# Performance work log

Measured on AMD Instinct MI355X. Metric: run time of the kernel, lower is better.

## Reference

```python
import jax, jax.numpy as jnp
import numpy as np

D = 20       # bond_dim (= virtual_dim = per-module output_dim)
BATCH = 128
BN_EPS = 1e-5


def _unfold(t, h, w, n):
    # torch x.unfold(2,h,h).unfold(3,w,w).reshape(b, C, -1, n)
    B, C, H, W = t.shape
    t = t.reshape(B, C, H // h, h, W // w, w).transpose(0, 1, 2, 4, 3, 5)
    return t.reshape(B, C, -1, n)


def _mps(x, cores, label):
    # x: [b, C, P, n] site values; cores: [P, n, D, F, D] with F = 2*C; label: [P, D, O, D]
    feat = jnp.concatenate([x, 1.0 - x], axis=1)              # [b, F, P, n]  ([x, 1-x] feature map)
    M = jnp.einsum('bfpn,pnufv->npbuv', feat, cores)           # [n, P, b, D, D] site matrices
    v = jnp.full((cores.shape[2],), cores.shape[2] ** -0.5, dtype=x.dtype)  # boundary vector
    left = jnp.einsum('u,pbuv->pbv', v, M[0])
    for i in range(1, M.shape[0]):                             # n is small & static (4 or 16)
        left = jnp.einsum('pbu,pbuv->pbv', left, M[i])
    return jnp.einsum('pbu,puov,v->bpo', left, label, v)       # [b, P, O]


def _bn(y, gamma, beta):
    # training-mode BatchNorm1d over channel axis 1 of [b, C, L]
    mean = y.mean(axis=(0, 2), keepdims=True)
    var = y.var(axis=(0, 2), keepdims=True)
    return (y - mean) * jax.lax.rsqrt(var + BN_EPS) * gamma[None, :, None] + beta[None, :, None]


def setup_inputs() -> dict:
    key = jax.random.key(0)
    ks = jax.random.split(key, 9)
    f32 = jnp.float32
    def core(k, shape):
        F = shape[-2]
        return (jax.random.normal(k, shape, f32) * np.float32(np.sqrt(3.0 / (D * F))))
    def lab(k, shape):
        return jax.random.normal(k, shape, f32) * np.float32(D ** -0.5)
    x = jax.random.uniform(ks[0], (BATCH, 48, 32, 32), f32)
    return {
        'x': x,
        'cores1': core(ks[1], (256, 4, D, 96, D)), 'label1': lab(ks[2], (256, D, D, D)),
        'g1': jnp.ones(256, f32), 'b1': jnp.zeros(256, f32),
        'cores2': core(ks[3], (64, 4, D, 2 * D, D)), 'label2': lab(ks[4], (64, D, D, D)),
        'g2': jnp.ones(64, f32), 'b2': jnp.zeros(64, f32),
        'cores3': core(ks[5], (16, 4, D, 2 * D, D)), 'label3': lab(ks[6], (16, D, D, D)),
        'g3': jnp.ones(16, f32), 'b3': jnp.zeros(16, f32),
        'coresF': core(ks[7], (16, D, 2 * D, D)), 'labelF': lab(ks[8], (D, 10, D)),
    }


def reference(x, cores1, label1, g1, b1, cores2, label2, g2, b2,
              cores3, label3, g3, b3, coresF, labelF):
    b = x.shape[0]
    # stage 1: 256 patch-experts over 4 sites each
    x1 = _unfold(x, 16, 16, 4)                  # [b, 48, 256, 4]
    y = _mps(x1, cores1, label1)                # [b, 256, D]
    y = _bn(y, g1, b1).reshape(b, D, 16, 16)    # faithful patch<->bond mixing view
    # stage 2: 64 experts
    y2 = _unfold(y, 8, 8, 4)                    # [b, D, 64, 4]
    y = _mps(y2, cores2, label2)                # [b, 64, D]
    y = _bn(y, g2, b2).reshape(b, D, 8, 8)
    # stage 3: 16 experts
    y3 = _unfold(y, 4, 4, 4)                    # [b, D, 16, 4]
    y = _mps(y3, cores3, label3)                # [b, 16, D]
    y = _bn(y, g3, b3)
    # final MPS over the 16 expert outputs (channels = D)
    y = y.transpose(0, 2, 1)[:, :, None, :]     # [b, D, 1, 16]
    out = _mps(y, coresF[None], labelF[None])   # [b, 1, 10]
    return out[:, 0, :]                         # squeeze -> [b, 10]
```

## Files before the change

### kernel.cpp

```cpp
#include <hip/hip_runtime.h>

#define VB 0.22360679774997896f

typedef __attribute__((ext_vector_type(8))) _Float16 half8;
typedef __attribute__((ext_vector_type(4))) float f32x4;

#define Z1_OFF   0
#define Z2_OFF   655360
#define Z3_OFF   819200
#define GS1_OFF  860160
#define GQ1_OFF  860416
#define GS2_OFF  860672
#define GQ2_OFF  860736
#define GS3_OFF  860800
#define GQ3_OFF  860816
#define LV1_OFF  860832
#define LV2_OFF  963232
#define LV3_OFF  988832
#define WH2_OFF  995232
#define WH3_OFF  4272032

#define WAVEBAR() __builtin_amdgcn_wave_barrier()

__global__ __launch_bounds__(256, 8)
void prep_kernel(const float* __restrict__ c2, const float* __restrict__ c3,
                 const float* __restrict__ l1, const float* __restrict__ l2,
                 const float* __restrict__ l3,
                 _Float16* __restrict__ Wh2, _Float16* __restrict__ Wh3,
                 float* __restrict__ v1, float* __restrict__ v2,
                 float* __restrict__ v3,
                 float* __restrict__ gzero)
{
    const int tid = threadIdx.x;
    const int b   = blockIdx.x;

    if (b < 4000) {
        int gidx = b * 256 + tid;
        int bb = gidx / 640;
        int o  = gidx - bb * 640;
        const float* src;
        _Float16* dst;
        if (bb < 1280) { src = c2 + (size_t)bb * 3200;          dst = Wh2 + (size_t)bb * 5120; }
        else           { src = c3 + (size_t)(bb - 1280) * 3200; dst = Wh3 + (size_t)(bb - 1280) * 5120; }
        int q  = o >> 6, l = o & 63;
        int ks = q / 5, nt = q - ks * 5;
        int c  = nt * 16 + (l & 15);
        int ul = c / 20;
        int v  = c - ul * 20;
        int f0 = ks * 32 + ((l >> 4) << 3);
        half8 hv;
        if (f0 < 40) {
            const float* sp = src + ul * 800 + f0 * 20 + v;
            #pragma unroll
            for (int j = 0; j < 8; ++j) hv[j] = (_Float16)sp[j * 20];
        } else {
            #pragma unroll
            for (int j = 0; j < 8; ++j) hv[j] = (_Float16)0.f;
        }
        *(half8*)(dst + (size_t)o * 8) = hv;
    } else if (b < 4336) {
        const int bb = b - 4000;
        const float* lb;
        float* ov;
        if (bb < 256)      { lb = l1 + (size_t)bb * 8000;         ov = v1 + bb * 400; }
        else if (bb < 320) { lb = l2 + (size_t)(bb - 256) * 8000; ov = v2 + (bb - 256) * 400; }
        else               { lb = l3 + (size_t)(bb - 320) * 8000; ov = v3 + (bb - 320) * 400; }
        for (int i = tid; i < 400; i += 256) {
            const float4* s = (const float4*)(lb + i * 20);
            float acc = 0.f;
            #pragma unroll
            for (int t = 0; t < 5; ++t) {
                float4 w = s[t];
                acc += w.x + w.y + w.z + w.w;
            }
            ov[i] = acc * VB;
        }
    } else {
        for (int i = tid; i < 672; i += 256) gzero[i] = 0.f;
    }
}

#define CHUNKX(ucv, LAST)                                                     \
    {                                                                         \
        if (!(LAST)) {                                                        \
            _Pragma("unroll")                                                 \
            for (int k = 0; k < 4; ++k) {                                     \
                int i4 = tid + k * 512;                                       \
                if (i4 < 1920) wr[k] = *(const float4*)(wnext + i4 * 4);      \
            }                                                                 \
            wnext += 7680;                                                    \
        }                                                                     \
        f32x4 acc[5];                                                         \
        _Pragma("unroll")                                                     \
        for (int nt = 0; nt < 5; ++nt) acc[nt] = (f32x4){0.f, 0.f, 0.f, 0.f};\
        _Pragma("unroll")                                                     \
        for (int ks = 0; ks < 3; ++ks) {                                      \
            _Pragma("unroll")                                                 \
            for (int nt = 0; nt < 5; ++nt) {                                  \
                half8 bf = *(const half8*)&Fcur[((ks * 5 + nt) * 64 + l) * 8];\
                acc[nt] = __builtin_amdgcn_mfma_f32_16x16x32_f16(             \
                    af[ks], bf, acc[nt], 0, 0, 0);                            \
            }                                                                 \
        }                                                                     \
        _Pragma("unroll")                                                     \
        for (int nt = 0; nt < 5; ++nt) {                                      \
            _Pragma("unroll")                                                 \
            for (int r = 0; r < 4; ++r)                                       \
                Mw[(hi * 4 + r) * 84 + nt * 16 + row16] = acc[nt][r];         \
        }                                                                     \
        WAVEBAR();                                                            \
        _Pragma("unroll")                                                     \
        for (int ul = 0; ul < 4; ++ul) {                                      \
            float lvx = lw[bQ * 20 + (ucv) * 4 + ul];                         \
            _Pragma("unroll")                                                 \
            for (int j = 0; j < 5; ++j)                                       \
                lacc[j] += lvx * Mw[bQ * 84 + ul * 20 + mh * 5 + j];          \
        }                                                                     \
        WAVEBAR();                                                            \
        __syncthreads();                                                      \
        if (!(LAST)) {                                                        \
            _Pragma("unroll")                                                 \
            for (int k = 0; k < 4; ++k) {                                     \
                int i4 = tid + k * 512;                                       \
                if (i4 < 1920) {                                              \
                    float vals[4] = {wr[k].x, wr[k].y, wr[k].z, wr[k].w};     \
                    _Pragma("unroll")                                         \
                    for (int t = 0; t < 4; ++t)                               \
                        Fnxt[sAddr[k][t]] = (_Float16)vals[t];                \
                }                                                             \
            }                                                                 \
        }                                                                     \
        __syncthreads();                                                      \
        { _Float16* t_ = Fcur; Fcur = Fnxt; Fnxt = t_; }                      \
    }

__global__ __launch_bounds__(512, 2)
void fused1_kernel(const float* __restrict__ x, const float* __restrict__ cores1,
                   const float* __restrict__ labv,
                   float* __restrict__ z1, float* __restrict__ gs, float* __restrict__ gq)
{
    __shared__ __align__(16) float xS[8 * 768];
    __shared__ __align__(16) _Float16 Fbuf[2][7680];
    __shared__ __align__(16) float MchunkS[8 * 16 * 84];
    __shared__ __align__(16) float leftS[8 * 320];
    __shared__ float redS[16];

    const int tid = threadIdx.x;
    const int bid = blockIdx.x;
    const int p   = (bid & 7) * 32 + (bid >> 3);
    const int wv  = tid >> 6, l = tid & 63;
    float* xSw = xS + wv * 768;
    float* Mw  = MchunkS + wv * 1344;
    float* lw  = leftS + wv * 320;
    const int row16 = l & 15, hi = l >> 4;
    const int bQ = l >> 2,   mh = l & 3;
    const int hh  = (p >> 7) * 16 + ((p >> 2) & 15);
    const int ww0 = ((p >> 6) & 1) * 16 + (p & 3) * 4;

    float4 xr[12];
    #pragma unroll
    for (int k = 0; k < 12; ++k) {
        int idx = l + k * 64;
        int br = idx / 48, c = idx - br * 48;
        xr[k] = *(const float4*)(x + (((size_t)((wv * 16 + br) * 48 + c)) << 10)
                                   + hh * 32 + ww0);
    }

    int sAddr[4][4];
    #pragma unroll
    for (int k = 0; k < 4; ++k) {
        int i4 = tid + k * 512;
        if (i4 < 1920) {
            #pragma unroll
            for (int t = 0; t < 4; ++t) {
                int e = i4 * 4 + t;
                int v = e % 20;
                int r = e / 20;
                int f = r % 96;
                int ul = r / 96;
                int c = ul * 20 + v;
                sAddr[k][t] = (((f >> 5) * 5 + (c >> 4)) * 64 +
                               ((f >> 3) & 3) * 16 + (c & 15)) * 8 + (f & 7);
            }
        }
    }

    #pragma unroll
    for (int j = 0; j < 5; ++j) lw[bQ * 20 + mh * 5 + j] = VB;
    WAVEBAR();

    float lacc[5] = {0.f, 0.f, 0.f, 0.f, 0.f};
    float4 wr[4];
    const float* wnext = cores1 + (size_t)p * 153600;

    #pragma unroll
    for (int k = 0; k < 4; ++k) {
        int i4 = tid + k * 512;
        if (i4 < 1920) wr[k] = *(const float4*)(wnext + i4 * 4);
    }
    wnext += 7680;
    _Float16* Fcur = &Fbuf[0][0];
    _Float16* Fnxt = &Fbuf[1][0];
    #pragma unroll
    for (int k = 0; k < 4; ++k) {
        int i4 = tid + k * 512;
        if (i4 < 1920) {
            float vals[4] = {wr[k].x, wr[k].y, wr[k].z, wr[k].w};
            #pragma unroll
            for (int t = 0; t < 4; ++t)
                Fcur[sAddr[k][t]] = (_Float16)vals[t];
        }
    }
    __syncthreads();

    #pragma unroll 1
    for (int n = 0; n < 4; ++n) {
        #pragma unroll
        for (int k = 0; k < 12; ++k) {
            int idx = l + k * 64;
            float v = (n == 0) ? xr[k].x : (n == 1) ? xr[k].y
                    : (n == 2) ? xr[k].z : xr[k].w;
            xSw[idx] = v;
        }
        WAVEBAR();
        half8 af[3];
        #pragma unroll
        for (int ks = 0; ks < 3; ++ks) {
            int f0 = ks * 32 + hi * 8;
            int cc = (f0 < 48) ? f0 : f0 - 48;
            float4 a  = *(const float4*)&xSw[row16 * 48 + cc];
            float4 b2 = *(const float4*)&xSw[row16 * 48 + cc + 4];
            float vv[8] = {a.x, a.y, a.z, a.w, b2.x, b2.y, b2.z, b2.w};
            bool inv = (f0 >= 48);
            half8 hv;
            #pragma unroll
            for (int j = 0; j < 8; ++j) hv[j] = (_Float16)(inv ? (1.f - vv[j]) : vv[j]);
            af[ks] = hv;
        }
        WAVEBAR();

        const bool last = (n == 3);
        CHUNKX(0, 0)
        CHUNKX(1, 0)
        CHUNKX(2, 0)
        CHUNKX(3, 0)
        CHUNKX(4, last)

        #pragma unroll
        for (int j = 0; j < 5; ++j) { lw[bQ * 20 + mh * 5 + j] = lacc[j]; lacc[j] = 0.f; }
        WAVEBAR();
    }

    const float* lvp = labv + p * 400;
    #pragma unroll
    for (int k = 0; k < 7; ++k) { int i = l + k * 64; if (i < 400) Mw[i] = lvp[i]; }
    WAVEBAR();
    float yv[5] = {0.f, 0.f, 0.f, 0.f, 0.f};
    #pragma unroll
    for (int u = 0; u < 20; ++u) {
        float lu = lw[bQ * 20 + u];
        #pragma unroll
        for (int j = 0; j < 5; ++j) yv[j] += lu * Mw[u * 20 + mh * 5 + j];
    }
    float s = 0.f, s2 = 0.f;
    #pragma unroll
    for (int j = 0; j < 5; ++j) {
        z1[(size_t)(wv * 16 + bQ) * 5120 + p * 20 + mh * 5 + j] = yv[j];
        s += yv[j]; s2 += yv[j] * yv[j];
    }
    #pragma unroll
    for (int off = 32; off > 0; off >>= 1) {
        s  += __shfl_down(s, off);
        s2 += __shfl_down(s2, off);
    }
    if (l == 0) { redS[wv] = s; redS[8 + wv] = s2; }
    __syncthreads();
    if (tid == 0) {
        float S = 0.f, Q = 0.f;
        #pragma unroll
        for (int w2 = 0; w2 < 8; ++w2) { S += redS[w2]; Q += redS[8 + w2]; }
        gs[p] = S; gq[p] = Q;
    }
}

#define UCBODYN(ucv, CUR, NXT)                                                   \
    {                                                                            \
        if ((ucv) < 4) {                                                         \
            const _Float16* bptr = whp + (size_t)((ucv) + 1) * 5120;             \
            _Pragma("unroll")                                                    \
            for (int q = 0; q < 10; ++q)                                         \
                NXT[q] = *(const half8*)(bptr + (q * 64 + l) * 8);               \
        }                                                                        \
        f32x4 acc[5];                                                            \
        _Pragma("unroll")                                                        \
        for (int nt = 0; nt < 5; ++nt) acc[nt] = (f32x4){0.f, 0.f, 0.f, 0.f};    \
        _Pragma("unroll")                                                        \
        for (int ks = 0; ks < 2; ++ks) {                                         \
            _Pragma("unroll")                                                    \
            for (int nt = 0; nt < 5; ++nt)                                       \
                acc[nt] = __builtin_amdgcn_mfma_f32_16x16x32_f16(                \
                    af[ks], CUR[ks * 5 + nt], acc[nt], 0, 0, 0);                 \
        }                                                                        \
        _Pragma("unroll")                                                        \
        for (int nt = 0; nt < 5; ++nt) {                                         \
            _Pragma("unroll")                                                    \
            for (int r = 0; r < 4; ++r)                                          \
                Mw[(hi * 4 + r) * 84 + nt * 16 + row16] = acc[nt][r];            \
        }                                                                        \
        WAVEBAR();                                                               \
        _Pragma("unroll")                                                        \
        for (int ul = 0; ul < 4; ++ul) {                                         \
            float lvx = lw[bQ * 20 + (ucv) * 4 + ul];                            \
            _Pragma("unroll")                                                    \
            for (int j = 0; j < 5; ++j)                                          \
                lacc[j] += lvx * Mw[bQ * 84 + ul * 20 + mh * 5 + j];             \
        }                                                                        \
        WAVEBAR();                                                               \
    }

template <int STAGE>
__global__ __launch_bounds__(256, 2)
void fusedN_kernel(const float* __restrict__ zin, const _Float16* __restrict__ Wh,
                   const float* __restrict__ labv,
                   const float* __restrict__ gsin, const float* __restrict__ gqin,
                   const float* __restrict__ gam,  const float* __restrict__ bet,
                   float* __restrict__ zout,
                   float* __restrict__ gsout, float* __restrict__ gqout)
{
    constexpr int ZIN  = (STAGE == 2) ? 5120 : 1280;
    constexpr int ZOUT = (STAGE == 2) ? 1280 : 320;
    constexpr int JUMP = (STAGE == 2) ? 256 : 64;

    __shared__ __align__(16) float zS[4 * 320];
    __shared__ float scS[4 * 20], shS[4 * 20];
    __shared__ __align__(16) float MchunkS[4 * 16 * 84];
    __shared__ __align__(16) float leftS[4 * 320];

    const int tid = threadIdx.x;
    const int p   = blockIdx.x;
    const int bh  = blockIdx.y;
    const int wv  = tid >> 6, l = tid & 63;
    float* zSw = zS + wv * 320;
    float* scw = scS + wv * 20;
    float* shw = shS + wv * 20;
    float* Mw  = MchunkS + wv * 1344;
    float* lw  = leftS + wv * 320;
    const int row16 = l & 15, hi = l >> 4;
    const int bQ = l >> 2,   mh = l & 3;
    const int bg = bh * 64;

    #pragma unroll
    for (int j = 0; j < 5; ++j) lw[bQ * 20 + mh * 5 + j] = VB;
    WAVEBAR();

    float lacc[5] = {0.f, 0.f, 0.f, 0.f, 0.f};

    #pragma unroll 1
    for (int n = 0; n < 4; ++n) {
        int hh, ww;
        if (STAGE == 2) { hh = (p >> 5) * 8 + ((p >> 1) & 7); ww = ((p >> 4) & 1) * 8 + (p & 1) * 4 + n; }
        else            { hh = (p >> 3) * 4 + (p & 3);        ww = ((p >> 2) & 1) * 4 + n; }
        const int oo = (STAGE == 2) ? (hh * 16 + ww) : (hh * 8 + ww);

        if (l < 20) {
            int ch = (l * JUMP + oo) / 20;
            float mean = gsin[ch] * (1.f / 2560.f);
            float var  = gqin[ch] * (1.f / 2560.f) - mean * mean;
            float rstd = rsqrtf(var + 1e-5f);
            float sc = gam[ch] * rstd;
            scw[l] = sc;
            shw[l] = bet[ch] - mean * sc;
        }
        WAVEBAR();
        #pragma unroll
        for (int q = 0; q < 5; ++q) {
            int d = hi * 5 + q;
            float zraw = zin[(size_t)(bg + wv * 16 + row16) * ZIN + d * JUMP + oo];
            zSw[row16 * 20 + d] = zraw * scw[d] + shw[d];
        }
        WAVEBAR();
        half8 af[2];
        #pragma unroll
        for (int ks = 0; ks < 2; ++ks) {
            int f0 = ks * 32 + hi * 8;
            half8 hv;
            #pragma unroll
            for (int j = 0; j < 8; ++j) {
                int f = f0 + j;
                float val;
                if (f < 20)      val = zSw[row16 * 20 + f];
                else if (f < 40) val = 1.f - zSw[row16 * 20 + f - 20];
                else             val = 0.f;
                hv[j] = (_Float16)val;
            }
            af[ks] = hv;
        }
        WAVEBAR();

        const _Float16* whp = Wh + (size_t)((p * 4 + n) * 5) * 5120;
        half8 bA[10], bB[10];
        {
            #pragma unroll
            for (int q = 0; q < 10; ++q) bA[q] = *(const half8*)(whp + (q * 64 + l) * 8);
        }
        UCBODYN(0, bA, bB)
        UCBODYN(1, bB, bA)
        UCBODYN(2, bA, bB)
        UCBODYN(3, bB, bA)
        UCBODYN(4, bA, bB)

        #pragma unroll
        for (int j = 0; j < 5; ++j) { lw[bQ * 20 + mh * 5 + j] = lacc[j]; lacc[j] = 0.f; }
        WAVEBAR();
    }

    const float* lvp = labv + p * 400;
    #pragma unroll
    for (int k = 0; k < 7; ++k) { int i = l + k * 64; if (i < 400) Mw[i] = lvp[i]; }
    WAVEBAR();
    float yv[5] = {0.f, 0.f, 0.f, 0.f, 0.f};
    #pragma unroll
    for (int u = 0; u < 20; ++u) {
        float lu = lw[bQ * 20 + u];
        #pragma unroll
        for (int j = 0; j < 5; ++j) yv[j] += lu * Mw[u * 20 + mh * 5 + j];
    }
    float s = 0.f, s2 = 0.f;
    #pragma unroll
    for (int j = 0; j < 5; ++j) {
        zout[(size_t)(bg + wv * 16 + bQ) * ZOUT + p * 20 + mh * 5 + j] = yv[j];
        s += yv[j]; s2 += yv[j] * yv[j];
    }
    #pragma unroll
    for (int off = 32; off > 0; off >>= 1) {
        s  += __shfl_down(s, off);
        s2 += __shfl_down(s2, off);
    }
    if (l == 0) { atomicAdd(&gsout[p], s); atomicAdd(&gqout[p], s2); }
}

__global__ __launch_bounds__(256, 4)
void final_kernel(const float* __restrict__ z3,
                  const float* __restrict__ coresF,
                  const float* __restrict__ labelF,
                  const float* __restrict__ g3,
                  const float* __restrict__ b3,
                  const float* __restrict__ gsum3,
                  const float* __restrict__ gsq3,
                  float* __restrict__ out)
{
    __shared__ __align__(16) float fS[16 * 40];
    __shared__ __align__(16) float MS[16 * 400];
    __shared__ float lvS[200];
    __shared__ float scS[16], shS[16];
    __shared__ float leftS[20];

    const int b   = blockIdx.x;
    const int tid = threadIdx.x;

    if (tid < 16) {
        float mean = gsum3[tid] * (1.f / 2560.f);
        float var  = gsq3[tid] * (1.f / 2560.f) - mean * mean;
        float rstd = rsqrtf(var + 1e-5f);
        float sc   = g3[tid] * rstd;
        scS[tid] = sc;
        shS[tid] = b3[tid] - mean * sc;
    }
    __syncthreads();

    for (int i = tid; i < 640; i += 256) {
        int n = i / 40, f = i - n * 40;
        float raw = z3[(size_t)b * 320 + n * 20 + (f % 20)];
        float val = raw * scS[n] + shS[n];
        fS[i] = (f < 20) ? val : (1.f - val);
    }
    for (int i = tid; i < 200; i += 256) {
        int u = i / 10, o = i - u * 10;
        const float* lb = labelF + (size_t)(u * 10 + o) * 20;
        float s = 0.f;
        #pragma unroll
        for (int vv = 0; vv < 20; ++vv) s += lb[vv];
        lvS[i] = s * VB;
    }
    __syncthreads();

    for (int i = tid; i < 6400; i += 256) {
        int n = i / 400, uv = i - n * 400;
        int u = uv / 20, v = uv - u * 20;
        const float* wb = coresF + ((size_t)(n * 20 + u) * 40) * 20 + v;
        const float* fb = fS + n * 40;
        float acc = 0.f;
        #pragma unroll
        for (int f = 0; f < 40; ++f) acc += fb[f] * wb[f * 20];
        MS[i] = acc;
    }
    __syncthreads();

    if (tid < 64) {
        if (tid < 20) leftS[tid] = VB;
        WAVEBAR();
        #pragma unroll 1
        for (int n = 0; n < 16; ++n) {
            float tmp = 0.f;
            if (tid < 20) {
                #pragma unroll
                for (int u = 0; u < 20; ++u) tmp += leftS[u] * MS[n * 400 + u * 20 + tid];
            }
            WAVEBAR();
            if (tid < 20) leftS[tid] = tmp;
            WAVEBAR();
        }
        if (tid < 10) {
            float s = 0.f;
            #pragma unroll
            for (int u = 0; u < 20; ++u) s += leftS[u] * lvS[u * 10 + tid];
            out[b * 10 + tid] = s;
        }
    }
}

extern "C" void kernel_launch(void* const* d_in, const int* in_sizes, int n_in,
                              void* d_out, int out_size, void* d_ws, size_t ws_size,
                              hipStream_t stream)
{
    const float* x      = (const float*)d_in[0];
    const float* cores1 = (const float*)d_in[1];
    const float* label1 = (const float*)d_in[2];
    const float* g1     = (const float*)d_in[3];
    const float* b1     = (const float*)d_in[4];
    const float* cores2 = (const float*)d_in[5];
    const float* label2 = (const float*)d_in[6];
    const float* g2     = (const float*)d_in[7];
    const float* b2     = (const float*)d_in[8];
    const float* cores3 = (const float*)d_in[9];
    const float* label3 = (const float*)d_in[10];
    const float* g3     = (const float*)d_in[11];
    const float* b3     = (const float*)d_in[12];
    const float* coresF = (const float*)d_in[13];
    const float* labelF = (const float*)d_in[14];

    float* ws  = (float*)d_ws;
    float* z1  = ws + Z1_OFF;
    float* z2  = ws + Z2_OFF;
    float* z3  = ws + Z3_OFF;
    float* gs1 = ws + GS1_OFF; float* gq1 = ws + GQ1_OFF;
    float* gs2 = ws + GS2_OFF; float* gq2 = ws + GQ2_OFF;
    float* gs3 = ws + GS3_OFF; float* gq3 = ws + GQ3_OFF;
    float* lv1 = ws + LV1_OFF;
    float* lv2 = ws + LV2_OFF;
    float* lv3 = ws + LV3_OFF;
    _Float16* Wh2 = (_Float16*)(ws + WH2_OFF);
    _Float16* Wh3 = (_Float16*)(ws + WH3_OFF);

    prep_kernel<<<4337, 256, 0, stream>>>(cores2, cores3,
                                          label1, label2, label3,
                                          Wh2, Wh3,
                                          lv1, lv2, lv3, gs1);

    fused1_kernel<<<256, 512, 0, stream>>>(x, cores1, lv1, z1, gs1, gq1);
    fusedN_kernel<2><<<dim3(64, 2), 256, 0, stream>>>(z1, Wh2, lv2, gs1, gq1, g1, b1,
                                                      z2, gs2, gq2);
    fusedN_kernel<3><<<dim3(16, 2), 256, 0, stream>>>(z2, Wh3, lv3, gs2, gq2, g2, b2,
                                                      z3, gs3, gq3);
    final_kernel<<<128, 256, 0, stream>>>(z3, coresF, labelF, g3, b3,
                                          gs3, gq3, (float*)d_out);
}
```

Baseline: 113.0 us.

## Merge all stages into one cooperative persistent kernel with grid syncs

Replaces the prep kernel and four stage launches with a single cooperative kernel of 256 blocks that runs stage 1, converts the stage 2/3 cores to fp16 inside the same launch, and separates later stages with grid.sync. Label reductions are now computed per block into LDS instead of in a separate prep pass. Stage 2/3 blocks now cover both batch halves with 512 threads and reduce statistics in LDS instead of using atomics. This is meant to remove launch gaps and the prep kernel. In exchange it adds grid-wide barrier cost, leaves most blocks idle in the later phases, and forces one block per CU because of the larger LDS footprint.

```diff
diff --git a/kernel.cpp b/kernel.cpp
--- a/kernel.cpp
+++ b/kernel.cpp
@@ -1,4 +1,7 @@
 #include <hip/hip_runtime.h>
+#include <hip/hip_cooperative_groups.h>
+
+namespace cg = cooperative_groups;
 
 #define VB 0.22360679774997896f
 
@@ -14,71 +17,23 @@
 #define GQ2_OFF  860736
 #define GS3_OFF  860800
 #define GQ3_OFF  860816
-#define LV1_OFF  860832
-#define LV2_OFF  963232
-#define LV3_OFF  988832
 #define WH2_OFF  995232
 #define WH3_OFF  4272032
 
 #define WAVEBAR() __builtin_amdgcn_wave_barrier()
 
-__global__ __launch_bounds__(256, 8)
-void prep_kernel(const float* __restrict__ c2, const float* __restrict__ c3,
-                 const float* __restrict__ l1, const float* __restrict__ l2,
-                 const float* __restrict__ l3,
-                 _Float16* __restrict__ Wh2, _Float16* __restrict__ Wh3,
-                 float* __restrict__ v1, float* __restrict__ v2,
-                 float* __restrict__ v3,
-                 float* __restrict__ gzero)
-{
-    const int tid = threadIdx.x;
-    const int b   = blockIdx.x;
-
-    if (b < 4000) {
-        int gidx = b * 256 + tid;
-        int bb = gidx / 640;
-        int o  = gidx - bb * 640;
-        const float* src;
-        _Float16* dst;
-        if (bb < 1280) { src = c2 + (size_t)bb * 3200;          dst = Wh2 + (size_t)bb * 5120; }
-        else           { src = c3 + (size_t)(bb - 1280) * 3200; dst = Wh3 + (size_t)(bb - 1280) * 5120; }
-        int q  = o >> 6, l = o & 63;
-        int ks = q / 5, nt = q - ks * 5;
-        int c  = nt * 16 + (l & 15);
-        int ul = c / 20;
-        int v  = c - ul * 20;
-        int f0 = ks * 32 + ((l >> 4) << 3);
-        half8 hv;
-        if (f0 < 40) {
-            const float* sp = src + ul * 800 + f0 * 20 + v;
-            #pragma unroll
-            for (int j = 0; j < 8; ++j) hv[j] = (_Float16)sp[j * 20];
-        } else {
-            #pragma unroll
-            for (int j = 0; j < 8; ++j) hv[j] = (_Float16)0.f;
-        }
-        *(half8*)(dst + (size_t)o * 8) = hv;
-    } else if (b < 4336) {
-        const int bb = b - 4000;
-        const float* lb;
-        float* ov;
-        if (bb < 256)      { lb = l1 + (size_t)bb * 8000;         ov = v1 + bb * 400; }
-        else if (bb < 320) { lb = l2 + (size_t)(bb - 256) * 8000; ov = v2 + (bb - 256) * 400; }
-        else               { lb = l3 + (size_t)(bb - 320) * 8000; ov = v3 + (bb - 320) * 400; }
-        for (int i = tid; i < 400; i += 256) {
-            const float4* s = (const float4*)(lb + i * 20);
-            float acc = 0.f;
-            #pragma unroll
-            for (int t = 0; t < 5; ++t) {
-                float4 w = s[t];
-                acc += w.x + w.y + w.z + w.w;
-            }
-            ov[i] = acc * VB;
-        }
-    } else {
-        for (int i = tid; i < 672; i += 256) gzero[i] = 0.f;
-    }
-}
+struct Args {
+    const float *x, *cores1, *label1, *g1, *b1;
+    const float *cores2, *label2, *g2, *b2;
+    const float *cores3, *label3, *g3, *b3;
+    const float *coresF, *labelF;
+    float *z1, *z2, *z3;
+    float *gs1, *gq1, *gs2, *gq2, *gs3, *gq3;
+    _Float16 *Wh2, *Wh3;
+    float *out;
+};
+
+#define LDS_BYTES 110208
 
 #define CHUNKX(ucv, LAST)                                                     \
     {                                                                         \
@@ -134,21 +89,19 @@
         { _Float16* t_ = Fcur; Fcur = Fnxt; Fnxt = t_; }                      \
     }
 
-__global__ __launch_bounds__(512, 2)
-void fused1_kernel(const float* __restrict__ x, const float* __restrict__ cores1,
-                   const float* __restrict__ labv,
-                   float* __restrict__ z1, float* __restrict__ gs, float* __restrict__ gq)
-{
-    __shared__ __align__(16) float xS[8 * 768];
-    __shared__ __align__(16) _Float16 Fbuf[2][7680];
-    __shared__ __align__(16) float MchunkS[8 * 16 * 84];
-    __shared__ __align__(16) float leftS[8 * 320];
-    __shared__ float redS[16];
-
-    const int tid = threadIdx.x;
-    const int bid = blockIdx.x;
-    const int p   = (bid & 7) * 32 + (bid >> 3);
-    const int wv  = tid >> 6, l = tid & 63;
+__device__ __forceinline__ void fused1_body(const Args& A, char* LDSU,
+                                            int bid, int tid)
+{
+    float*     xS      = (float*)LDSU;
+    _Float16*  Fb0     = (_Float16*)(LDSU + 24576);
+    _Float16*  Fb1     = (_Float16*)(LDSU + 39936);
+    float*     MchunkS = (float*)(LDSU + 55296);
+    float*     leftS   = (float*)(LDSU + 98304);
+    float*     labvS   = (float*)(LDSU + 108544);
+    float*     redS    = (float*)(LDSU + 110144);
+
+    const int p  = (bid & 7) * 32 + (bid >> 3);
+    const int wv = tid >> 6, l = tid & 63;
     float* xSw = xS + wv * 768;
     float* Mw  = MchunkS + wv * 1344;
     float* lw  = leftS + wv * 320;
@@ -162,7 +115,7 @@
     for (int k = 0; k < 12; ++k) {
         int idx = l + k * 64;
         int br = idx / 48, c = idx - br * 48;
-        xr[k] = *(const float4*)(x + (((size_t)((wv * 16 + br) * 48 + c)) << 10)
+        xr[k] = *(const float4*)(A.x + (((size_t)((wv * 16 + br) * 48 + c)) << 10)
                                    + hh * 32 + ww0);
     }
 
@@ -191,7 +144,7 @@
 
     float lacc[5] = {0.f, 0.f, 0.f, 0.f, 0.f};
     float4 wr[4];
-    const float* wnext = cores1 + (size_t)p * 153600;
+    const float* wnext = A.cores1 + (size_t)p * 153600;
 
     #pragma unroll
     for (int k = 0; k < 4; ++k) {
@@ -199,8 +152,8 @@
         if (i4 < 1920) wr[k] = *(const float4*)(wnext + i4 * 4);
     }
     wnext += 7680;
-    _Float16* Fcur = &Fbuf[0][0];
-    _Float16* Fnxt = &Fbuf[1][0];
+    _Float16* Fcur = Fb0;
+    _Float16* Fnxt = Fb1;
     #pragma unroll
     for (int k = 0; k < 4; ++k) {
         int i4 = tid + k * 512;
@@ -212,6 +165,14 @@
         }
     }
     __syncthreads();
+
+    if (tid < 400) {
+        const float* lb = A.label1 + (size_t)p * 8000 + tid * 20;
+        float s = 0.f;
+        #pragma unroll
+        for (int vv = 0; vv < 20; ++vv) s += lb[vv];
+        labvS[tid] = s * VB;
+    }
 
     #pragma unroll 1
     for (int n = 0; n < 4; ++n) {
@@ -251,21 +212,17 @@
         WAVEBAR();
     }
 
-    const float* lvp = labv + p * 400;
-    #pragma unroll
-    for (int k = 0; k < 7; ++k) { int i = l + k * 64; if (i < 400) Mw[i] = lvp[i]; }
-    WAVEBAR();
     float yv[5] = {0.f, 0.f, 0.f, 0.f, 0.f};
     #pragma unroll
     for (int u = 0; u < 20; ++u) {
         float lu = lw[bQ * 20 + u];
         #pragma unroll
-        for (int j = 0; j < 5; ++j) yv[j] += lu * Mw[u * 20 + mh * 5 + j];
+        for (int j = 0; j < 5; ++j) yv[j] += lu * labvS[u * 20 + mh * 5 + j];
     }
     float s = 0.f, s2 = 0.f;
     #pragma unroll
     for (int j = 0; j < 5; ++j) {
-        z1[(size_t)(wv * 16 + bQ) * 5120 + p * 20 + mh * 5 + j] = yv[j];
+        A.z1[(size_t)(wv * 16 + bQ) * 5120 + p * 20 + mh * 5 + j] = yv[j];
         s += yv[j]; s2 += yv[j] * yv[j];
     }
     #pragma unroll
@@ -279,7 +236,35 @@
         float S = 0.f, Q = 0.f;
         #pragma unroll
         for (int w2 = 0; w2 < 8; ++w2) { S += redS[w2]; Q += redS[8 + w2]; }
-        gs[p] = S; gq[p] = Q;
+        A.gs1[p] = S; A.gq1[p] = Q;
+    }
+}
+
+__device__ __forceinline__ void wconv_slice(const Args& A, int bid, int tid)
+{
+    for (int i = bid * 512 + tid; i < 1024000; i += 131072) {
+        int bb = i / 640;
+        int o  = i - bb * 640;
+        const float* src;
+        _Float16* dst;
+        if (bb < 1280) { src = A.cores2 + (size_t)bb * 3200;          dst = A.Wh2 + (size_t)bb * 5120; }
+        else           { src = A.cores3 + (size_t)(bb - 1280) * 3200; dst = A.Wh3 + (size_t)(bb - 1280) * 5120; }
+        int q  = o >> 6, l2 = o & 63;
+        int ks = q / 5, nt = q - ks * 5;
+        int c  = nt * 16 + (l2 & 15);
+        int ul = c / 20;
+        int v  = c - ul * 20;
+        int f0 = ks * 32 + ((l2 >> 4) << 3);
+        half8 hv;
+        if (f0 < 40) {
+            const float* sp = src + ul * 800 + f0 * 20 + v;
+            #pragma unroll
+            for (int j = 0; j < 8; ++j) hv[j] = (_Float16)sp[j * 20];
+        } else {
+            #pragma unroll
+            for (int j = 0; j < 8; ++j) hv[j] = (_Float16)0.f;
+        }
+        *(half8*)(dst + (size_t)o * 8) = hv;
     }
 }
 
@@ -319,27 +304,37 @@
     }
 
 template <int STAGE>
-__global__ __launch_bounds__(256, 2)
-void fusedN_kernel(const float* __restrict__ zin, const _Float16* __restrict__ Wh,
-                   const float* __restrict__ labv,
-                   const float* __restrict__ gsin, const float* __restrict__ gqin,
-                   const float* __restrict__ gam,  const float* __restrict__ bet,
-                   float* __restrict__ zout,
-                   float* __restrict__ gsout, float* __restrict__ gqout)
-{
+__device__ __forceinline__ void stageN_phase(const Args& A, char* LDSU,
+                                             int bid, int tid)
+{
+    constexpr int PC   = (STAGE == 2) ? 64 : 16;
     constexpr int ZIN  = (STAGE == 2) ? 5120 : 1280;
     constexpr int ZOUT = (STAGE == 2) ? 1280 : 320;
     constexpr int JUMP = (STAGE == 2) ? 256 : 64;
-
-    __shared__ __align__(16) float zS[4 * 320];
-    __shared__ float scS[4 * 20], shS[4 * 20];
-    __shared__ __align__(16) float MchunkS[4 * 16 * 84];
-    __shared__ __align__(16) float leftS[4 * 320];
-
-    const int tid = threadIdx.x;
-    const int p   = blockIdx.x;
-    const int bh  = blockIdx.y;
-    const int wv  = tid >> 6, l = tid & 63;
+    if (bid >= PC) return;
+
+    float* zS      = (float*)LDSU;
+    float* scS     = (float*)(LDSU + 10240);
+    float* shS     = (float*)(LDSU + 10880);
+    float* MchunkS = (float*)(LDSU + 11520);
+    float* leftS   = (float*)(LDSU + 54528);
+    float* labvS   = (float*)(LDSU + 64768);
+    float* redS    = (float*)(LDSU + 66368);
+
+    const float*   zin   = (STAGE == 2) ? A.z1 : A.z2;
+    const _Float16* Wh   = (STAGE == 2) ? A.Wh2 : A.Wh3;
+    const float*   label = (STAGE == 2) ? A.label2 : A.label3;
+    const float*   gsin  = (STAGE == 2) ? A.gs1 : A.gs2;
+    const float*   gqin  = (STAGE == 2) ? A.gq1 : A.gq2;
+    const float*   gam   = (STAGE == 2) ? A.g1 : A.g2;
+    const float*   bet   = (STAGE == 2) ? A.b1 : A.b2;
+    float*         zout  = (STAGE == 2) ? A.z2 : A.z3;
+    float*         gsout = (STAGE == 2) ? A.gs2 : A.gs3;
+    float*         gqout = (STAGE == 2) ? A.gq2 : A.gq3;
+
+    const int p  = bid;
+    const int wv = tid >> 6, l = tid & 63;
+    const int bh = wv >> 2, wvl = wv & 3;
     float* zSw = zS + wv * 320;
     float* scw = scS + wv * 20;
     float* shw = shS + wv * 20;
@@ -347,7 +342,16 @@
     float* lw  = leftS + wv * 320;
     const int row16 = l & 15, hi = l >> 4;
     const int bQ = l >> 2,   mh = l & 3;
-    const int bg = bh * 64;
+    const int bg = bh * 64 + wvl * 16;
+
+    if (tid < 400) {
+        const float* lb = label + (size_t)p * 8000 + tid * 20;
+        float s = 0.f;
+        #pragma unroll
+        for (int vv = 0; vv < 20; ++vv) s += lb[vv];
+        labvS[tid] = s * VB;
+    }
+    __syncthreads();
 
     #pragma unroll
     for (int j = 0; j < 5; ++j) lw[bQ * 20 + mh * 5 + j] = VB;
@@ -375,7 +379,7 @@
         #pragma unroll
         for (int q = 0; q < 5; ++q) {
             int d = hi * 5 + q;
-            float zraw = zin[(size_t)(bg + wv * 16 + row16) * ZIN + d * JUMP + oo];
+            float zraw = zin[(size_t)(bg + row16) * ZIN + d * JUMP + oo];
             zSw[row16 * 20 + d] = zraw * scw[d] + shw[d];
         }
         WAVEBAR();
@@ -414,21 +418,17 @@
         WAVEBAR();
     }
 
-    const float* lvp = labv + p * 400;
-    #pragma unroll
-    for (int k = 0; k < 7; ++k) { int i = l + k * 64; if (i < 400) Mw[i] = lvp[i]; }
-    WAVEBAR();
     float yv[5] = {0.f, 0.f, 0.f, 0.f, 0.f};
     #pragma unroll
     for (int u = 0; u < 20; ++u) {
         float lu = lw[bQ * 20 + u];
         #pragma unroll
-        for (int j = 0; j < 5; ++j) yv[j] += lu * Mw[u * 20 + mh * 5 + j];
+        for (int j = 0; j < 5; ++j) yv[j] += lu * labvS[u * 20 + mh * 5 + j];
     }
     float s = 0.f, s2 = 0.f;
     #pragma unroll
     for (int j = 0; j < 5; ++j) {
-        zout[(size_t)(bg + wv * 16 + bQ) * ZOUT + p * 20 + mh * 5 + j] = yv[j];
+        zout[(size_t)(bg + bQ) * ZOUT + p * 20 + mh * 5 + j] = yv[j];
         s += yv[j]; s2 += yv[j] * yv[j];
     }
     #pragma unroll
@@ -436,47 +436,48 @@
         s  += __shfl_down(s, off);
         s2 += __shfl_down(s2, off);
     }
-    if (l == 0) { atomicAdd(&gsout[p], s); atomicAdd(&gqout[p], s2); }
-}
-
-__global__ __launch_bounds__(256, 4)
-void final_kernel(const float* __restrict__ z3,
-                  const float* __restrict__ coresF,
-                  const float* __restrict__ labelF,
-                  const float* __restrict__ g3,
-                  const float* __restrict__ b3,
-                  const float* __restrict__ gsum3,
-                  const float* __restrict__ gsq3,
-                  float* __restrict__ out)
-{
-    __shared__ __align__(16) float fS[16 * 40];
-    __shared__ __align__(16) float MS[16 * 400];
-    __shared__ float lvS[200];
-    __shared__ float scS[16], shS[16];
-    __shared__ float leftS[20];
-
-    const int b   = blockIdx.x;
-    const int tid = threadIdx.x;
+    if (l == 0) { redS[wv] = s; redS[8 + wv] = s2; }
+    __syncthreads();
+    if (tid == 0) {
+        float S = 0.f, Q = 0.f;
+        #pragma unroll
+        for (int w2 = 0; w2 < 8; ++w2) { S += redS[w2]; Q += redS[8 + w2]; }
+        gsout[p] = S; gqout[p] = Q;
+    }
+}
+
+__device__ __forceinline__ void final_phase(const Args& A, char* LDSU,
+                                            int bid, int tid)
+{
+    if (bid >= 128) return;
+    float* fS    = (float*)LDSU;
+    float* MS    = (float*)(LDSU + 2560);
+    float* lvS   = (float*)(LDSU + 28160);
+    float* scS   = (float*)(LDSU + 28960);
+    float* shS   = (float*)(LDSU + 29024);
+    float* leftS = (float*)(LDSU + 29088);
+
+    const int b = bid;
 
     if (tid < 16) {
-        float mean = gsum3[tid] * (1.f / 2560.f);
-        float var  = gsq3[tid] * (1.f / 2560.f) - mean * mean;
+        float mean = A.gs3[tid] * (1.f / 2560.f);
+        float var  = A.gq3[tid] * (1.f / 2560.f) - mean * mean;
         float rstd = rsqrtf(var + 1e-5f);
-        float sc   = g3[tid] * rstd;
+        float sc   = A.g3[tid] * rstd;
         scS[tid] = sc;
-        shS[tid] = b3[tid] - mean * sc;
+        shS[tid] = A.b3[tid] - mean * sc;
     }
     __syncthreads();
 
-    for (int i = tid; i < 640; i += 256) {
+    for (int i = tid; i < 640; i += 512) {
         int n = i / 40, f = i - n * 40;
-        float raw = z3[(size_t)b * 320 + n * 20 + (f % 20)];
+        float raw = A.z3[(size_t)b * 320 + n * 20 + (f % 20)];
         float val = raw * scS[n] + shS[n];
         fS[i] = (f < 20) ? val : (1.f - val);
     }
-    for (int i = tid; i < 200; i += 256) {
+    for (int i = tid; i < 200; i += 512) {
         int u = i / 10, o = i - u * 10;
-        const float* lb = labelF + (size_t)(u * 10 + o) * 20;
+        const float* lb = A.labelF + (size_t)(u * 10 + o) * 20;
         float s = 0.f;
         #pragma unroll
         for (int vv = 0; vv < 20; ++vv) s += lb[vv];
@@ -484,10 +485,10 @@
     }
     __syncthreads();
 
-    for (int i = tid; i < 6400; i += 256) {
+    for (int i = tid; i < 6400; i += 512) {
         int n = i / 400, uv = i - n * 400;
         int u = uv / 20, v = uv - u * 20;
-        const float* wb = coresF + ((size_t)(n * 20 + u) * 40) * 20 + v;
+        const float* wb = A.coresF + ((size_t)(n * 20 + u) * 40) * 20 + v;
         const float* fb = fS + n * 40;
         float acc = 0.f;
         #pragma unroll
@@ -514,54 +515,97 @@
             float s = 0.f;
             #pragma unroll
             for (int u = 0; u < 20; ++u) s += leftS[u] * lvS[u * 10 + tid];
-            out[b * 10 + tid] = s;
-        }
-    }
+            A.out[b * 10 + tid] = s;
+        }
+    }
+}
+
+__global__ __launch_bounds__(512, 1)
+void mega_kernel(Args A)
+{
+    __shared__ __align__(16) char LDSU[LDS_BYTES];
+    const int tid = threadIdx.x;
+    const int bid = blockIdx.x;
+    cg::grid_group grid = cg::this_grid();
+
+    fused1_body(A, LDSU, bid, tid);
+    wconv_slice(A, bid, tid);
+    grid.sync();
+    stageN_phase<2>(A, LDSU, bid, tid);
+    grid.sync();
+    stageN_phase<3>(A, LDSU, bid, tid);
+    grid.sync();
+    final_phase(A, LDSU, bid, tid);
+}
+
+__global__ __launch_bounds__(512, 1)
+void k_fused1(Args A)
+{
+    __shared__ __align__(16) char LDSU[LDS_BYTES];
+    fused1_body(A, LDSU, blockIdx.x, threadIdx.x);
+    wconv_slice(A, blockIdx.x, threadIdx.x);
+}
+
+__global__ __launch_bounds__(512, 1)
+void k_stage2(Args A)
+{
+    __shared__ __align__(16) char LDSU[LDS_BYTES];
+    stageN_phase<2>(A, LDSU, blockIdx.x, threadIdx.x);
+}
+
+__global__ __launch_bounds__(512, 1)
+void k_stage3(Args A)
+{
+    __shared__ __align__(16) char LDSU[LDS_BYTES];
+    stageN_phase<3>(A, LDSU, blockIdx.x, threadIdx.x);
+}
+
+__global__ __launch_bounds__(512, 1)
+void k_final(Args A)
+{
+    __shared__ __align__(16) char LDSU[LDS_BYTES];
+    final_phase(A, LDSU, blockIdx.x, threadIdx.x);
 }
 
 extern "C" void kernel_launch(void* const* d_in, const int* in_sizes, int n_in,
                               void* d_out, int out_size, void* d_ws, size_t ws_size,
                               hipStream_t stream)
 {
-    const float* x      = (const float*)d_in[0];
-    const float* cores1 = (const float*)d_in[1];
-    const float* label1 = (const float*)d_in[2];
-    const float* g1     = (const float*)d_in[3];
-    const float* b1     = (const float*)d_in[4];
-    const float* cores2 = (const float*)d_in[5];
-    const float* label2 = (const float*)d_in[6];
-    const float* g2     = (const float*)d_in[7];
-    const float* b2     = (const float*)d_in[8];
-    const float* cores3 = (const float*)d_in[9];
-    const float* label3 = (const float*)d_in[10];
-    const float* g3     = (const float*)d_in[11];
-    const float* b3     = (const float*)d_in[12];
-    const float* coresF = (const float*)d_in[13];
-    const float* labelF = (const float*)d_in[14];
-
-    float* ws  = (float*)d_ws;
-    float* z1  = ws + Z1_OFF;
-    float* z2  = ws + Z2_OFF;
-    float* z3  = ws + Z3_OFF;
-    float* gs1 = ws + GS1_OFF; float* gq1 = ws + GQ1_OFF;
-    float* gs2 = ws + GS2_OFF; float* gq2 = ws + GQ2_OFF;
-    float* gs3 = ws + GS3_OFF; float* gq3 = ws + GQ3_OFF;
-    float* lv1 = ws + LV1_OFF;
-    float* lv2 = ws + LV2_OFF;
-    float* lv3 = ws + LV3_OFF;
-    _Float16* Wh2 = (_Float16*)(ws + WH2_OFF);
-    _Float16* Wh3 = (_Float16*)(ws + WH3_OFF);
-
-    prep_kernel<<<4337, 256, 0, stream>>>(cores2, cores3,
-                                          label1, label2, label3,
-                                          Wh2, Wh3,
-                                          lv1, lv2, lv3, gs1);
-
-    fused1_kernel<<<256, 512, 0, stream>>>(x, cores1, lv1, z1, gs1, gq1);
-    fusedN_kernel<2><<<dim3(64, 2), 256, 0, stream>>>(z1, Wh2, lv2, gs1, gq1, g1, b1,
-                                                      z2, gs2, gq2);
-    fusedN_kernel<3><<<dim3(16, 2), 256, 0, stream>>>(z2, Wh3, lv3, gs2, gq2, g2, b2,
-                                                      z3, gs3, gq3);
-    final_kernel<<<128, 256, 0, stream>>>(z3, coresF, labelF, g3, b3,
-                                          gs3, gq3, (float*)d_out);
-}
+    float* ws = (float*)d_ws;
+    Args A;
+    A.x      = (const float*)d_in[0];
+    A.cores1 = (const float*)d_in[1];
+    A.label1 = (const float*)d_in[2];
+    A.g1     = (const float*)d_in[3];
+    A.b1     = (const float*)d_in[4];
+    A.cores2 = (const float*)d_in[5];
+    A.label2 = (const float*)d_in[6];
+    A.g2     = (const float*)d_in[7];
+    A.b2     = (const float*)d_in[8];
+    A.cores3 = (const float*)d_in[9];
+    A.label3 = (const float*)d_in[10];
+    A.g3     = (const float*)d_in[11];
+    A.b3     = (const float*)d_in[12];
+    A.coresF = (const float*)d_in[13];
+    A.labelF = (const float*)d_in[14];
+    A.z1  = ws + Z1_OFF;
+    A.z2  = ws + Z2_OFF;
+    A.z3  = ws + Z3_OFF;
+    A.gs1 = ws + GS1_OFF; A.gq1 = ws + GQ1_OFF;
+    A.gs2 = ws + GS2_OFF; A.gq2 = ws + GQ2_OFF;
+    A.gs3 = ws + GS3_OFF; A.gq3 = ws + GQ3_OFF;
+    A.Wh2 = (_Float16*)(ws + WH2_OFF);
+    A.Wh3 = (_Float16*)(ws + WH3_OFF);
+    A.out = (float*)d_out;
+
+    void* kargs[] = {&A};
+    hipError_t err = hipLaunchCooperativeKernel((void*)mega_kernel,
+                                                dim3(256), dim3(512),
+                                                kargs, 0, stream);
+    if (err != hipSuccess) {
+        k_fused1<<<256, 512, 0, stream>>>(A);
+        k_stage2<<<64, 512, 0, stream>>>(A);
+        k_stage3<<<16, 512, 0, stream>>>(A);
+        k_final<<<128, 512, 0, stream>>>(A);
+    }
+}
```

New measurement: 230.9 us. 104% more time.
